# Kernel optimization log

Measured on AMD Instinct MI355X. Metric: run time of the kernel, lower is better.

## Reference

```python
import jax, jax.numpy as jnp
import numpy as np
from functools import partial

B = 1024          # batch of VRP instances
N_CUST = 100      # customers
N = N_CUST + 1    # nodes incl. depot (node 0)
E = 128           # embed_dim
H = 8             # n_heads
DH = E // H       # head depth
CLIP = 10.0
T = 2 * N         # fixed number of decode steps (env.n_nodes * 2)


def setup_inputs() -> dict:
    key = jax.random.key(0)
    ks = jax.random.split(key, 11)
    s = E ** -0.5
    return {
        "depot_xy": jax.random.uniform(ks[0], (B, 2), dtype=jnp.float32),
        "customer_xy": jax.random.uniform(ks[1], (B, N_CUST, 2), dtype=jnp.float32),
        # demands normalized by vehicle capacity (1..9 / 50 for VRP100)
        "demand": jax.random.uniform(ks[2], (B, N_CUST), dtype=jnp.float32, minval=0.02, maxval=0.18),
        "node_embeddings": jax.random.normal(ks[3], (B, N, E), dtype=jnp.float32),
        "graph_embedding": jax.random.normal(ks[4], (B, E), dtype=jnp.float32),
        "Wk1": jax.random.normal(ks[5], (E, E), dtype=jnp.float32) * s,
        "Wv": jax.random.normal(ks[6], (E, E), dtype=jnp.float32) * s,
        "Wk2": jax.random.normal(ks[7], (E, E), dtype=jnp.float32) * s,
        "Wq_fixed": jax.random.normal(ks[8], (E, E), dtype=jnp.float32) * s,
        "Wout": jax.random.normal(ks[9], (E, E), dtype=jnp.float32) * s,
        "Wq_step": jax.random.normal(ks[10], (E + 1, E), dtype=jnp.float32) * s,
    }


def _decode(depot_xy, customer_xy, demand, node_embeddings, graph_embedding,
            Wk1, Wv, Wk2, Wq_fixed, Wout, Wq_step):
    # ---- compute_static ----
    Q_fixed = jnp.einsum('be,ef->bf', graph_embedding, Wq_fixed)[:, None, :]  # [B,1,E]
    K1 = jnp.einsum('bne,ef->bnf', node_embeddings, Wk1)                      # [B,N,E]
    V  = jnp.einsum('bne,ef->bnf', node_embeddings, Wv)
    K2 = jnp.einsum('bne,ef->bnf', node_embeddings, Wk2)
    K1h = K1.reshape(B, N, H, DH)
    Vh  = V.reshape(B, N, H, DH)
    inv_sqrt_dh = 1.0 / np.sqrt(DH)
    inv_sqrt_e = 1.0 / np.sqrt(E)
    bidx = jnp.arange(B)
    NEG = jnp.float32(-1e9)

    def step(carry, _):
        mask, D, prev_node, visited = carry
        # step_context = [embedding of current node, remaining capacity D]
        prev_emb = node_embeddings[bidx, prev_node]                 # [B,E]
        step_context = jnp.concatenate([prev_emb, D], axis=-1)[:, None, :]  # [B,1,E+1]
        # ---- compute_dynamic ----
        Q1 = Q_fixed + jnp.einsum('bqc,cf->bqf', step_context, Wq_step)      # [B,1,E]
        Q1h = Q1.reshape(B, 1, H, DH)
        scores = jnp.einsum('bqhd,bkhd->bhqk', Q1h, K1h) * inv_sqrt_dh       # [B,H,1,N]
        scores = jnp.where(mask[:, None, None, :], NEG, scores)
        attn = jax.nn.softmax(scores, axis=-1)
        glimpse = jnp.einsum('bhqk,bkhd->bqhd', attn, Vh).reshape(B, 1, E)
        Q2 = jnp.einsum('bqe,ef->bqf', glimpse, Wout)                        # [B,1,E]
        logits = CLIP * jnp.tanh(jnp.einsum('bqe,bke->bqk', Q2, K2) * inv_sqrt_e)
        logits = jnp.where(mask[:, None, :], NEG, logits)[:, 0]             # [B,N]
        log_p = jax.nn.log_softmax(logits, axis=-1)
        next_node = jnp.argmax(log_p, axis=-1)                               # greedy decode
        # ---- env._get_step ----
        is_depot = next_node == 0
        cust = jnp.clip(next_node - 1, 0, N_CUST - 1)
        sel_dem = jnp.where(is_depot, 0.0, demand[bidx, cust])
        D_new = jnp.where(is_depot[:, None], 1.0, D - sel_dem[:, None])      # refill at depot
        sel_onehot = (jnp.arange(N_CUST)[None, :] == cust[:, None]) & (~is_depot[:, None])
        visited = visited | sel_onehot
        mask_cust = visited | (demand > D_new)                               # visited or too big
        all_visited = jnp.all(visited, axis=-1)
        mask_depot = is_depot & (~all_visited)                               # can't stay at depot
        mask = jnp.concatenate([mask_depot[:, None], mask_cust], axis=-1)
        return (mask, D_new, next_node, visited), (log_p, next_node)

    mask0 = jnp.concatenate([jnp.ones((B, 1), bool), jnp.zeros((B, N_CUST), bool)], axis=-1)
    D0 = jnp.ones((B, 1), jnp.float32)
    prev0 = jnp.zeros((B,), jnp.int32)
    visited0 = jnp.zeros((B, N_CUST), bool)
    _, (log_ps, tours) = jax.lax.scan(step, (mask0, D0, prev0, visited0), None, length=T)
    log_ps = jnp.transpose(log_ps, (1, 0, 2))   # [B,T,N]
    tours = jnp.transpose(tours, (1, 0))        # [B,T]

    # ---- get_costs ----
    coords = jnp.concatenate([depot_xy[:, None, :], customer_xy], axis=1)    # [B,N,2]
    d = coords[bidx[:, None], tours]                                         # [B,T,2]
    def seglen(v):
        return jnp.sqrt(jnp.sum(v * v, axis=-1) + 1e-10)
    cost = (seglen(d[:, 1:] - d[:, :-1]).sum(-1)
            + seglen(d[:, 0] - depot_xy) + seglen(d[:, -1] - depot_xy))
    # ---- get_log_likelihood ----
    ll = jnp.take_along_axis(log_ps, tours[..., None], axis=-1)[..., 0].sum(-1)
    return cost, ll


def reference(depot_xy, customer_xy, demand, node_embeddings, graph_embedding,
              Wk1, Wv, Wk2, Wq_fixed, Wout, Wq_step):
    return _decode(depot_xy, customer_xy, demand, node_embeddings, graph_embedding,
                   Wk1, Wv, Wk2, Wq_fixed, Wout, Wq_step)
```

## Files before the change

### kernel.cpp

```cpp
#include <hip/hip_runtime.h>
#include <math.h>

#define B_   1024
#define NC   100
#define NN   101
#define E_   128
#define T_   202
#define SVP  132
#define NEGV   -1.0e9
#define GAPTHR 1.0e-3f
#define INVSQE 0.08838834764831845f
#define INVSQED 0.08838834764831845

__device__ __forceinline__ float rdlane(float v, int l) {
    return __int_as_float(__builtin_amdgcn_readlane(__float_as_int(v), l));
}
__device__ __forceinline__ float fast_tanh(float x) {
    float xc = fminf(fmaxf(x, -15.f), 15.f);
    float e  = __expf(2.f * xc);
    return (e - 1.f) / (e + 1.f);
}

__global__ void k_weights(const float* __restrict__ Wk2,
                          const float* __restrict__ Wout,
                          double* __restrict__ M64,
                          float* __restrict__ M32) {
    int g = blockIdx.x;
    int e = threadIdx.x;
    const float* w2 = Wk2 + g * E_;
    const float* wo = Wout + e * E_;
    double acc = 0.0;
#pragma unroll 8
    for (int f = 0; f < E_; ++f) acc += (double)w2[f] * (double)wo[f];
    M64[g * E_ + e] = acc;
    M32[g * E_ + e] = (float)acc;
}

__global__ __launch_bounds__(512, 2)
void k_decode(const float* __restrict__ depot_xy,
              const float* __restrict__ customer_xy,
              const float* __restrict__ demand,
              const float* __restrict__ node_emb,
              const float* __restrict__ graph_emb,
              const float* __restrict__ Wk1,
              const float* __restrict__ Wv,
              const float* __restrict__ Wq_fixed,
              const float* __restrict__ Wq_step,
              const double* __restrict__ M64,
              const float* __restrict__ M32,
              float* __restrict__ out)
{
    __shared__ float  sKs[NN * E_];
    __shared__ __align__(16) float sV[104 * SVP];
    __shared__ double sU[2224];
    __shared__ double sQfix64[E_];
    __shared__ double sWqD64[E_];
    __shared__ float  sQfix32[E_];
    __shared__ float  sWqD32[E_];
    __shared__ float  sCoord[2 * NN];
    __shared__ float  sDem[NC];
    __shared__ float  sD;
    __shared__ double sCost, sLL;
    __shared__ float  sPosX, sPosY;
    __shared__ int    sPrev, sMaskDepot, sTrig, sOvf;
    __shared__ unsigned long long sVis0, sVis1;

    float* fSc = (float*)sU;
    float* gl  = (float*)sU + 832;
    float* fPx = (float*)sU + 960;
    double* dUZ = sU;
    double* dSc = sU + 1024;
    double* dQ1 = sU + 1832;
    double* dGl = sU + 1960;
    double* dVg = sU + 2088;

    const int b      = blockIdx.x;
    const int tid    = threadIdx.x;
    const int lane   = tid & 63;
    const int h      = __builtin_amdgcn_readfirstlane(tid >> 6);
    const int k1     = lane + 64;
    const int k_lane = tid & 127;
    const int q2u    = __builtin_amdgcn_readfirstlane(tid >> 7);
    const int e0     = q2u * 32;

    const float* emb = node_emb + (size_t)b * NN * E_;

    if (tid < E_) {
        const float* ge = graph_emb + (size_t)b * E_;
        double acc = 0.0;
        for (int g = 0; g < E_; ++g)
            acc += (double)ge[g] * (double)Wq_fixed[g * E_ + tid];
        sQfix64[tid] = acc;
        sQfix32[tid] = (float)acc;
        sWqD64[tid]  = (double)Wq_step[128 * E_ + tid];
        sWqD32[tid]  = Wq_step[128 * E_ + tid];
    }
    if (tid < 2 * NN) {
        int k = tid >> 1, xy = tid & 1;
        sCoord[tid] = (k == 0) ? depot_xy[(size_t)b * 2 + xy]
                               : customer_xy[((size_t)b * NC + (k - 1)) * 2 + xy];
    }
    if (tid < NC) sDem[tid] = demand[(size_t)b * NC + tid];
    if (tid == 0) {
        sD = 1.f; sPrev = 0; sVis0 = 0ull; sVis1 = 0ull;
        sMaskDepot = 1; sCost = 0.0; sLL = 0.0; sTrig = 0; sOvf = 0;
        sPosX = depot_xy[(size_t)b * 2 + 0];
        sPosY = depot_xy[(size_t)b * 2 + 1];
    }
    for (int i = tid; i < 3 * SVP; i += 512) sV[101 * SVP + i] = 0.f;

    for (int idx = tid; idx < NN * 32; idx += 512) {
        int k  = idx >> 5;
        int e4 = (idx & 31) * 4;
        const float* er = emb + (size_t)k * E_;
        float4 aV = {0.f, 0.f, 0.f, 0.f};
        float4 aK = {0.f, 0.f, 0.f, 0.f};
        for (int g = 0; g < E_; ++g) {
            float eg = er[g];
            float4 wv = *(const float4*)(Wv      + (size_t)g * E_ + e4);
            float4 wq = *(const float4*)(Wq_step + (size_t)g * E_ + e4);
            aV.x += eg * wv.x; aV.y += eg * wv.y;
            aV.z += eg * wv.z; aV.w += eg * wv.w;
            aK.x += eg * wq.x; aK.y += eg * wq.y;
            aK.z += eg * wq.z; aK.w += eg * wq.w;
        }
        *(float4*)(sV  + (size_t)k * SVP + e4) = aV;
        *(float4*)(sKs + (size_t)k * E_  + e4) = aK;
    }

    float rA[32];
#pragma unroll
    for (int j = 0; j < 32; ++j) rA[j] = 0.f;
    {
        const float* er0 = emb + (size_t)lane * E_;
        const float* er1 = emb + (size_t)((k1 < NN) ? k1 : lane) * E_;
        const float  e1s = (k1 < NN) ? 1.f : 0.f;
        const float* w1b = Wk1 + h * 16;
        for (int g = 0; g < E_; ++g) {
            float a0 = er0[g];
            float a1 = er1[g] * e1s;
            const float* w1 = w1b + (size_t)g * E_;
#pragma unroll
            for (int d = 0; d < 16; ++d) {
                rA[d]      += a0 * w1[d];
                rA[16 + d] += a1 * w1[d];
            }
        }
    }

    float rK2[32];
#pragma unroll
    for (int j = 0; j < 32; ++j) rK2[j] = 0.f;
    if (k_lane < NN) {
        const float* er = emb + (size_t)k_lane * E_;
        for (int g = 0; g < E_; ++g) {
            float eg = er[g];
            const float* mm = M32 + (size_t)g * E_ + e0;
#pragma unroll
            for (int j = 0; j < 32; ++j) rK2[j] += eg * mm[j];
        }
    }
    __syncthreads();

    for (int t = 0; t < T_; ++t) {
        {
            int prev = sPrev;
            float Dv = sD;
            int d_ = h * 16 + (lane & 15);
            float q1v = (sQfix32[d_] + sKs[(size_t)prev * E_ + d_]
                         + Dv * sWqD32[d_]) * 0.25f;

            unsigned long long v0 = sVis0, v1 = sVis1;
            bool mk0, mk1;
            if (lane == 0) mk0 = (sMaskDepot != 0);
            else {
                int c = lane - 1;
                mk0 = ((v0 >> c) & 1ull) || (sDem[c] > Dv);
            }
            if (k1 < NN) {
                int c = k1 - 1;
                bool vis = (c < 64) ? ((v0 >> c) & 1ull)
                                    : ((v1 >> (c - 64)) & 1ull);
                mk1 = vis || (sDem[c] > Dv);
            } else mk1 = true;

            float s0a = 0.f, s0b = 0.f, s1a = 0.f, s1b = 0.f;
#pragma unroll
            for (int d = 0; d < 8; ++d) {
                float qd = rdlane(q1v, d);
                s0a += rA[d] * qd;
                s1a += rA[16 + d] * qd;
            }
#pragma unroll
            for (int d = 8; d < 16; ++d) {
                float qd = rdlane(q1v, d);
                s0b += rA[d] * qd;
                s1b += rA[16 + d] * qd;
            }
            float s0 = s0a + s0b, s1 = s1a + s1b;
            bool ovf = (!mk0 && s0 > 80.f) || (!mk1 && s1 > 80.f);
            if (__any(ovf)) { if (lane == 0) sOvf = 1; }
            float w0 = mk0 ? 0.f : __expf(fminf(s0, 80.f));
            float w1 = mk1 ? 0.f : __expf(fminf(s1, 80.f));
            fSc[h * 104 + lane] = w0;
            if (k1 < 104) fSc[h * 104 + k1] = w1;

            __builtin_amdgcn_wave_barrier();

            int cq4 = lane >> 4;
            const float* sc = fSc + h * 104 + cq4 * 26;
            const float* vv = sV + (size_t)(cq4 * 26) * SVP + d_;
            float p = 0.f, ssum = 0.f;
#pragma unroll
            for (int j = 0; j < 26; ++j) {
                float wgt = sc[j];
                p    += wgt * vv[(size_t)j * SVP];
                ssum += wgt;
            }
            p    += __shfl_xor(p, 16);
            ssum += __shfl_xor(ssum, 16);
            p    += __shfl_xor(p, 32);
            ssum += __shfl_xor(ssum, 32);
            if (lane < 16) gl[d_] = p * (1.0f / ssum);
        }
        __syncthreads();

        {
            int ee = e0 + (tid & 31);
            float glv = gl[ee];
            float xa = 0.f, xb = 0.f, xc = 0.f, xd = 0.f;
#pragma unroll
            for (int j = 0; j < 8; ++j)   xa += rK2[j] * rdlane(glv, j);
#pragma unroll
            for (int j = 8; j < 16; ++j)  xb += rK2[j] * rdlane(glv, j);
#pragma unroll
            for (int j = 16; j < 24; ++j) xc += rK2[j] * rdlane(glv, j);
#pragma unroll
            for (int j = 24; j < 32; ++j) xd += rK2[j] * rdlane(glv, j);
            if (k_lane < NN) fPx[q2u * E_ + k_lane] = (xa + xb) + (xc + xd);
        }
        __syncthreads();

        if (tid < 64) {
            int kA = tid, kB = tid + 64;
            float xA = (fPx[kA] + fPx[128 + kA] + fPx[256 + kA] + fPx[384 + kA]) * INVSQE;
            bool mk1;
            if (kA == 0) mk1 = (sMaskDepot != 0);
            else {
                int c = kA - 1;
                bool vis = (c < 64) ? ((sVis0 >> c) & 1ull) : ((sVis1 >> (c - 64)) & 1ull);
                mk1 = vis || (sDem[c] > sD);
            }
            float xB = -3.0e38f; bool mk2 = true;
            if (kB < NN) {
                xB = (fPx[kB] + fPx[128 + kB] + fPx[256 + kB] + fPx[384 + kB]) * INVSQE;
                int c = kB - 1;
                bool vis = (c < 64) ? ((sVis0 >> c) & 1ull) : ((sVis1 >> (c - 64)) & 1ull);
                mk2 = vis || (sDem[c] > sD);
            }
            float a1v = mk1 ? -3.0e38f : xA;
            float a2v = mk2 ? -3.0e38f : xB;
            float m1; int mi;
            if (a2v > a1v) { m1 = a2v; mi = kB; }
            else           { m1 = a1v; mi = kA; }
            float ls = 0.f;
            if (!mk1)              ls += __expf(10.f * fast_tanh(xA));
            if (kB < NN && !mk2)   ls += __expf(10.f * fast_tanh(xB));
#pragma unroll
            for (int off = 32; off > 0; off >>= 1) {
                float om1 = __shfl_xor(m1, off);
                int   omi = __shfl_xor(mi, off);
                ls += __shfl_xor(ls, off);
                if (om1 > m1 || (om1 == m1 && omi < mi)) { m1 = om1; mi = omi; }
            }
            bool near = false;
            if (!mk1 && kA != mi && a1v > m1 - GAPTHR) near = true;
            if (!mk2 && kB != mi && a2v > m1 - GAPTHR) near = true;
            bool trigAny = __any(near);
            if (tid == 0) {
                bool trig = trigAny || (sOvf != 0) || !(m1 == m1);
                sOvf = 0;
                if (trig) {
                    sTrig = 1;
                } else {
                    float lsel = 10.f * fast_tanh(m1);
                    float logp = lsel - __logf(ls);
                    int nxt = mi;
                    sLL += (double)logp;
                    bool isdep = (nxt == 0);
                    if (isdep) {
                        sD = 1.0f;
                    } else {
                        int c = nxt - 1;
                        sD = sD - sDem[c];
                        if (c < 64) sVis0 |= (1ull << c);
                        else        sVis1 |= (1ull << (c - 64));
                    }
                    bool allv = (sVis0 == 0xFFFFFFFFFFFFFFFFull) &&
                                (sVis1 == 0x0000000FFFFFFFFFull);
                    sMaskDepot = (isdep && !allv) ? 1 : 0;
                    sPrev = nxt;
                    float cx = sCoord[2 * nxt], cy = sCoord[2 * nxt + 1];
                    double dx = (double)cx - (double)sPosX;
                    double dy = (double)cy - (double)sPosY;
                    sCost += sqrt(dx * dx + dy * dy + 1e-10);
                    sPosX = cx; sPosY = cy;
                }
            }
        }
        __syncthreads();

        if (sTrig) {
            if (tid < E_) {
                const float* ep = emb + (size_t)sPrev * E_;
                double ks = 0.0;
                for (int g = 0; g < E_; ++g)
                    ks += (double)ep[g] * (double)Wq_step[(size_t)g * E_ + tid];
                dQ1[tid] = (sQfix64[tid] + ks + (double)sD * sWqD64[tid]) * 0.25;
            }
            __syncthreads();
            for (int idx = tid; idx < 1024; idx += 512) {
                int g = idx >> 3, hh = idx & 7;
                double u = 0.0;
#pragma unroll 4
                for (int d = 0; d < 16; ++d)
                    u += dQ1[hh * 16 + d] * (double)Wk1[(size_t)g * E_ + hh * 16 + d];
                dUZ[idx] = u;
            }
            __syncthreads();
            for (int idx = tid; idx < 1024; idx += 512) {
                int k = idx & 127, hh = idx >> 7;
                if (k < NN) {
                    bool mk;
                    if (k == 0) mk = (sMaskDepot != 0);
                    else {
                        int c = k - 1;
                        bool vis = (c < 64) ? ((sVis0 >> c) & 1ull) : ((sVis1 >> (c - 64)) & 1ull);
                        mk = vis || (sDem[c] > sD);
                    }
                    if (mk) dSc[hh * NN + k] = NEGV;
                    else {
                        const float* ek = emb + (size_t)k * E_;
                        double s = 0.0;
                        for (int g = 0; g < E_; ++g)
                            s += (double)ek[g] * dUZ[g * 8 + hh];
                        dSc[hh * NN + k] = s;
                    }
                }
            }
            __syncthreads();
            {
                int hh = tid >> 6, ln = tid & 63;
                int kA = ln, kB = ln + 64;
                double v1 = dSc[hh * NN + kA];
                double v2 = (kB < NN) ? dSc[hh * NN + kB] : -1.0e300;
                double m = fmax(v1, v2);
#pragma unroll
                for (int off = 32; off > 0; off >>= 1)
                    m = fmax(m, __shfl_xor(m, off));
                double e1 = exp(v1 - m);
                double e2 = (kB < NN) ? exp(v2 - m) : 0.0;
                double s = e1 + e2;
#pragma unroll
                for (int off = 32; off > 0; off >>= 1)
                    s += __shfl_xor(s, off);
                double inv = 1.0 / s;
                dSc[hh * NN + kA] = e1 * inv;
                if (kB < NN) dSc[hh * NN + kB] = e2 * inv;
            }
            __syncthreads();
            for (int idx = tid; idx < 1024; idx += 512) {
                int g = idx >> 3, hh = idx & 7;
                double z = 0.0;
                for (int k = 0; k < NN; ++k)
                    z += dSc[hh * NN + k] * (double)emb[(size_t)k * E_ + g];
                dUZ[idx] = z;
            }
            __syncthreads();
            if (tid < E_) {
                int hh = tid >> 4;
                double g2 = 0.0;
                for (int g = 0; g < E_; ++g)
                    g2 += dUZ[g * 8 + hh] * (double)Wv[(size_t)g * E_ + tid];
                dGl[tid] = g2;
            }
            __syncthreads();
            if (tid < E_) {
                double v = 0.0;
                for (int e = 0; e < E_; ++e)
                    v += dGl[e] * M64[(size_t)tid * E_ + e];
                dVg[tid] = v;
            }
            __syncthreads();
            if (tid < NN) {
                const float* ek = emb + (size_t)tid * E_;
                double x = 0.0;
                for (int g = 0; g < E_; ++g)
                    x += (double)ek[g] * dVg[g];
                dQ1[tid] = x * INVSQED;
            }
            __syncthreads();
            if (tid < 64) {
                int kA = tid, kB = tid + 64;
                double x1 = dQ1[kA];
                bool mk1;
                if (kA == 0) mk1 = (sMaskDepot != 0);
                else {
                    int c = kA - 1;
                    bool vis = (c < 64) ? ((sVis0 >> c) & 1ull) : ((sVis1 >> (c - 64)) & 1ull);
                    mk1 = vis || (sDem[c] > sD);
                }
                double x2 = 0.0; bool mk2 = true;
                if (kB < NN) {
                    x2 = dQ1[kB];
                    int c = kB - 1;
                    bool vis = (c < 64) ? ((sVis0 >> c) & 1ull) : ((sVis1 >> (c - 64)) & 1ull);
                    mk2 = vis || (sDem[c] > sD);
                }
                double a1 = mk1 ? -1.0e300 : x1;
                double a2 = (kB < NN && !mk2) ? x2 : -1.0e300;
                double mv; int mi;
                if (a1 >= a2) { mv = a1; mi = kA; } else { mv = a2; mi = kB; }
#pragma unroll
                for (int off = 32; off > 0; off >>= 1) {
                    double ov = __shfl_xor(mv, off);
                    int    oi = __shfl_xor(mi, off);
                    if (ov > mv || (ov == mv && oi < mi)) { mv = ov; mi = oi; }
                }
                double lmax = 10.0 * tanh(mv);
                double l1 = mk1 ? NEGV : 10.0 * tanh(x1);
                double l2 = (kB < NN) ? (mk2 ? NEGV : 10.0 * tanh(x2)) : 0.0;
                double s = exp(l1 - lmax) + ((kB < NN) ? exp(l2 - lmax) : 0.0);
#pragma unroll
                for (int off = 32; off > 0; off >>= 1)
                    s += __shfl_xor(s, off);
                if (tid == 0) {
                    int nxt = mi;
                    sLL += -log(s);
                    bool isdep = (nxt == 0);
                    if (isdep) {
                        sD = 1.0f;
                    } else {
                        int c = nxt - 1;
                        sD = sD - sDem[c];
                        if (c < 64) sVis0 |= (1ull << c);
                        else        sVis1 |= (1ull << (c - 64));
                    }
                    bool allv = (sVis0 == 0xFFFFFFFFFFFFFFFFull) &&
                                (sVis1 == 0x0000000FFFFFFFFFull);
                    sMaskDepot = (isdep && !allv) ? 1 : 0;
                    sPrev = nxt;
                    float cx = sCoord[2 * nxt], cy = sCoord[2 * nxt + 1];
                    double dx = (double)cx - (double)sPosX;
                    double dy = (double)cy - (double)sPosY;
                    sCost += sqrt(dx * dx + dy * dy + 1e-10);
                    sPosX = cx; sPosY = cy;
                    sTrig = 0;
                }
            }
            __syncthreads();
        }
    }

    if (tid == 0) {
        double dx = (double)sCoord[0] - (double)sPosX;
        double dy = (double)sCoord[1] - (double)sPosY;
        out[b]      = (float)(sCost + sqrt(dx * dx + dy * dy + 1e-10));
        out[B_ + b] = (float)sLL;
    }
}

extern "C" void kernel_launch(void* const* d_in, const int* in_sizes, int n_in,
                              void* d_out, int out_size, void* d_ws, size_t ws_size,
                              hipStream_t stream) {
    const float* depot = (const float*)d_in[0];
    const float* cust  = (const float*)d_in[1];
    const float* dem   = (const float*)d_in[2];
    const float* nemb  = (const float*)d_in[3];
    const float* gemb  = (const float*)d_in[4];
    const float* Wk1   = (const float*)d_in[5];
    const float* Wv    = (const float*)d_in[6];
    const float* Wk2   = (const float*)d_in[7];
    const float* Wqf   = (const float*)d_in[8];
    const float* Wout  = (const float*)d_in[9];
    const float* Wqs   = (const float*)d_in[10];
    float*  out = (float*)d_out;
    double* M64 = (double*)d_ws;
    float*  M32 = (float*)((char*)d_ws + 131072);

    k_weights<<<dim3(128), dim3(128), 0, stream>>>(Wk2, Wout, M64, M32);
    k_decode <<<dim3(B_),  dim3(512), 0, stream>>>(depot, cust, dem, nemb, gemb,
                                                   Wk1, Wv, Wqf, Wqs, M64, M32, out);
}
```

Before: 3.197 ms.

## Shrink LDS footprint to raise occupancy by moving Ks table to global workspace

Moves the per-node Ks projection table out of shared memory into a global workspace buffer and removes the double-precision shared buffers. The rare fp64 fallback step moves into a noinline device function that reuses the sV region as scratch and rebuilds sV afterwards. Launch bounds go from 2 to 4 blocks per CU so more batch blocks can be resident. In exchange, each step now reads Ks from global memory, and the fallback does extra recomputation. The old kernel is kept for when the workspace is too small.

```diff
diff --git a/kernel.cpp b/kernel.cpp
--- a/kernel.cpp
+++ b/kernel.cpp
@@ -36,25 +36,217 @@
     M32[g * E_ + e] = (float)acc;
 }
 
-__global__ __launch_bounds__(512, 2)
-void k_decode(const float* __restrict__ depot_xy,
-              const float* __restrict__ customer_xy,
-              const float* __restrict__ demand,
-              const float* __restrict__ node_emb,
-              const float* __restrict__ graph_emb,
-              const float* __restrict__ Wk1,
-              const float* __restrict__ Wv,
-              const float* __restrict__ Wq_fixed,
-              const float* __restrict__ Wq_step,
-              const double* __restrict__ M64,
-              const float* __restrict__ M32,
-              float* __restrict__ out)
+__device__ __attribute__((noinline)) void fb_step(
+    const float* __restrict__ emb,
+    const float* __restrict__ gemb_b,
+    const float* __restrict__ Wk1,
+    const float* __restrict__ Wv,
+    const float* __restrict__ Wq_fixed,
+    const float* __restrict__ Wq_step,
+    const double* __restrict__ M64,
+    float* sV,
+    const float* sDem, const float* sCoord,
+    float* sD, int* sPrev, int* sMaskDepot,
+    unsigned long long* sVis0, unsigned long long* sVis1,
+    double* sCost, double* sLL, float* sPosX, float* sPosY,
+    int* sTrig, int tid)
 {
-    __shared__ float  sKs[NN * E_];
+    double* dUZ = (double*)sV;
+    double* dSc = dUZ + 1024;
+    double* dQ1 = dUZ + 1832;
+    double* dGl = dUZ + 1960;
+    double* dVg = dUZ + 2088;
+
+    if (tid < E_) {
+        double qf = 0.0, ks = 0.0;
+        const float* ep = emb + (size_t)(*sPrev) * E_;
+#pragma clang loop unroll(disable)
+        for (int g = 0; g < E_; ++g) {
+            qf += (double)gemb_b[g] * (double)Wq_fixed[(size_t)g * E_ + tid];
+            ks += (double)ep[g]     * (double)Wq_step[(size_t)g * E_ + tid];
+        }
+        dQ1[tid] = (qf + ks + (double)(*sD) * (double)Wq_step[128 * E_ + tid]) * 0.25;
+    }
+    __syncthreads();
+    for (int idx = tid; idx < 1024; idx += 512) {
+        int g = idx >> 3, hh = idx & 7;
+        double u = 0.0;
+#pragma clang loop unroll(disable)
+        for (int d = 0; d < 16; ++d)
+            u += dQ1[hh * 16 + d] * (double)Wk1[(size_t)g * E_ + hh * 16 + d];
+        dUZ[idx] = u;
+    }
+    __syncthreads();
+    for (int idx = tid; idx < 1024; idx += 512) {
+        int k = idx & 127, hh = idx >> 7;
+        if (k < NN) {
+            bool mk;
+            if (k == 0) mk = (*sMaskDepot != 0);
+            else {
+                int c = k - 1;
+                bool vis = (c < 64) ? ((*sVis0 >> c) & 1ull) : ((*sVis1 >> (c - 64)) & 1ull);
+                mk = vis || (sDem[c] > *sD);
+            }
+            if (mk) dSc[hh * NN + k] = NEGV;
+            else {
+                const float* ek = emb + (size_t)k * E_;
+                double s = 0.0;
+#pragma clang loop unroll(disable)
+                for (int g = 0; g < E_; ++g)
+                    s += (double)ek[g] * dUZ[g * 8 + hh];
+                dSc[hh * NN + k] = s;
+            }
+        }
+    }
+    __syncthreads();
+    {
+        int hh = tid >> 6, ln = tid & 63;
+        int kA = ln, kB = ln + 64;
+        double v1 = dSc[hh * NN + kA];
+        double v2 = (kB < NN) ? dSc[hh * NN + kB] : -1.0e300;
+        double m = fmax(v1, v2);
+#pragma unroll
+        for (int off = 32; off > 0; off >>= 1)
+            m = fmax(m, __shfl_xor(m, off));
+        double e1 = exp(v1 - m);
+        double e2 = (kB < NN) ? exp(v2 - m) : 0.0;
+        double s = e1 + e2;
+#pragma unroll
+        for (int off = 32; off > 0; off >>= 1)
+            s += __shfl_xor(s, off);
+        double inv = 1.0 / s;
+        dSc[hh * NN + kA] = e1 * inv;
+        if (kB < NN) dSc[hh * NN + kB] = e2 * inv;
+    }
+    __syncthreads();
+    for (int idx = tid; idx < 1024; idx += 512) {
+        int g = idx >> 3, hh = idx & 7;
+        double z = 0.0;
+#pragma clang loop unroll(disable)
+        for (int k = 0; k < NN; ++k)
+            z += dSc[hh * NN + k] * (double)emb[(size_t)k * E_ + g];
+        dUZ[idx] = z;
+    }
+    __syncthreads();
+    if (tid < E_) {
+        int hh = tid >> 4;
+        double g2 = 0.0;
+#pragma clang loop unroll(disable)
+        for (int g = 0; g < E_; ++g)
+            g2 += dUZ[g * 8 + hh] * (double)Wv[(size_t)g * E_ + tid];
+        dGl[tid] = g2;
+    }
+    __syncthreads();
+    if (tid < E_) {
+        double v = 0.0;
+#pragma clang loop unroll(disable)
+        for (int e = 0; e < E_; ++e)
+            v += dGl[e] * M64[(size_t)tid * E_ + e];
+        dVg[tid] = v;
+    }
+    __syncthreads();
+    if (tid < NN) {
+        const float* ek = emb + (size_t)tid * E_;
+        double x = 0.0;
+#pragma clang loop unroll(disable)
+        for (int g = 0; g < E_; ++g)
+            x += (double)ek[g] * dVg[g];
+        dQ1[tid] = x * INVSQED;
+    }
+    __syncthreads();
+    if (tid < 64) {
+        int kA = tid, kB = tid + 64;
+        double x1 = dQ1[kA];
+        bool mk1;
+        if (kA == 0) mk1 = (*sMaskDepot != 0);
+        else {
+            int c = kA - 1;
+            bool vis = (c < 64) ? ((*sVis0 >> c) & 1ull) : ((*sVis1 >> (c - 64)) & 1ull);
+            mk1 = vis || (sDem[c] > *sD);
+        }
+        double x2 = 0.0; bool mk2 = true;
+        if (kB < NN) {
+            x2 = dQ1[kB];
+            int c = kB - 1;
+            bool vis = (c < 64) ? ((*sVis0 >> c) & 1ull) : ((*sVis1 >> (c - 64)) & 1ull);
+            mk2 = vis || (sDem[c] > *sD);
+        }
+        double a1 = mk1 ? -1.0e300 : x1;
+        double a2 = (kB < NN && !mk2) ? x2 : -1.0e300;
+        double mv; int mi;
+        if (a1 >= a2) { mv = a1; mi = kA; } else { mv = a2; mi = kB; }
+#pragma unroll
+        for (int off = 32; off > 0; off >>= 1) {
+            double ov = __shfl_xor(mv, off);
+            int    oi = __shfl_xor(mi, off);
+            if (ov > mv || (ov == mv && oi < mi)) { mv = ov; mi = oi; }
+        }
+        double lmax = 10.0 * tanh(mv);
+        double l1 = mk1 ? NEGV : 10.0 * tanh(x1);
+        double l2 = (kB < NN) ? (mk2 ? NEGV : 10.0 * tanh(x2)) : 0.0;
+        double s = exp(l1 - lmax) + ((kB < NN) ? exp(l2 - lmax) : 0.0);
+#pragma unroll
+        for (int off = 32; off > 0; off >>= 1)
+            s += __shfl_xor(s, off);
+        if (tid == 0) {
+            int nxt = mi;
+            *sLL += -log(s);
+            bool isdep = (nxt == 0);
+            if (isdep) {
+                *sD = 1.0f;
+            } else {
+                int c = nxt - 1;
+                *sD = *sD - sDem[c];
+                if (c < 64) *sVis0 |= (1ull << c);
+                else        *sVis1 |= (1ull << (c - 64));
+            }
+            bool allv = (*sVis0 == 0xFFFFFFFFFFFFFFFFull) &&
+                        (*sVis1 == 0x0000000FFFFFFFFFull);
+            *sMaskDepot = (isdep && !allv) ? 1 : 0;
+            *sPrev = nxt;
+            float cx = sCoord[2 * nxt], cy = sCoord[2 * nxt + 1];
+            double dx = (double)cx - (double)(*sPosX);
+            double dy = (double)cy - (double)(*sPosY);
+            *sCost += sqrt(dx * dx + dy * dy + 1e-10);
+            *sPosX = cx; *sPosY = cy;
+            *sTrig = 0;
+        }
+    }
+    __syncthreads();
+
+    for (int idx = tid; idx < NN * 32; idx += 512) {
+        int k  = idx >> 5;
+        int e4 = (idx & 31) * 4;
+        const float* er = emb + (size_t)k * E_;
+        float4 aV = {0.f, 0.f, 0.f, 0.f};
+#pragma clang loop unroll(disable)
+        for (int g = 0; g < E_; ++g) {
+            float eg = er[g];
+            float4 wv = *(const float4*)(Wv + (size_t)g * E_ + e4);
+            aV.x += eg * wv.x; aV.y += eg * wv.y;
+            aV.z += eg * wv.z; aV.w += eg * wv.w;
+        }
+        *(float4*)(sV + (size_t)k * SVP + e4) = aV;
+    }
+}
+
+__global__ __launch_bounds__(512, 4)
+void k_decode_g(const float* __restrict__ depot_xy,
+                const float* __restrict__ customer_xy,
+                const float* __restrict__ demand,
+                const float* __restrict__ node_emb,
+                const float* __restrict__ graph_emb,
+                const float* __restrict__ Wk1,
+                const float* __restrict__ Wv,
+                const float* __restrict__ Wq_fixed,
+                const float* __restrict__ Wq_step,
+                const double* __restrict__ M64,
+                const float* __restrict__ M32,
+                float* __restrict__ gks,
+                float* __restrict__ out)
+{
     __shared__ __align__(16) float sV[104 * SVP];
-    __shared__ double sU[2224];
-    __shared__ double sQfix64[E_];
-    __shared__ double sWqD64[E_];
+    __shared__ float  sF[1472];
     __shared__ float  sQfix32[E_];
     __shared__ float  sWqD32[E_];
     __shared__ float  sCoord[2 * NN];
@@ -65,14 +257,9 @@
     __shared__ int    sPrev, sMaskDepot, sTrig, sOvf;
     __shared__ unsigned long long sVis0, sVis1;
 
-    float* fSc = (float*)sU;
-    float* gl  = (float*)sU + 832;
-    float* fPx = (float*)sU + 960;
-    double* dUZ = sU;
-    double* dSc = sU + 1024;
-    double* dQ1 = sU + 1832;
-    double* dGl = sU + 1960;
-    double* dVg = sU + 2088;
+    float* fSc = sF;
+    float* gl  = sF + 832;
+    float* fPx = sF + 960;
 
     const int b      = blockIdx.x;
     const int tid    = threadIdx.x;
@@ -83,16 +270,14 @@
     const int q2u    = __builtin_amdgcn_readfirstlane(tid >> 7);
     const int e0     = q2u * 32;
 
-    const float* emb = node_emb + (size_t)b * NN * E_;
+    const float* emb    = node_emb + (size_t)b * NN * E_;
+    const float* gemb_b = graph_emb + (size_t)b * E_;
 
     if (tid < E_) {
-        const float* ge = graph_emb + (size_t)b * E_;
         double acc = 0.0;
         for (int g = 0; g < E_; ++g)
-            acc += (double)ge[g] * (double)Wq_fixed[g * E_ + tid];
-        sQfix64[tid] = acc;
+            acc += (double)gemb_b[g] * (double)Wq_fixed[g * E_ + tid];
         sQfix32[tid] = (float)acc;
-        sWqD64[tid]  = (double)Wq_step[128 * E_ + tid];
         sWqD32[tid]  = Wq_step[128 * E_ + tid];
     }
     if (tid < 2 * NN) {
@@ -124,8 +309,8 @@
             aK.x += eg * wq.x; aK.y += eg * wq.y;
             aK.z += eg * wq.z; aK.w += eg * wq.w;
         }
-        *(float4*)(sV  + (size_t)k * SVP + e4) = aV;
-        *(float4*)(sKs + (size_t)k * E_  + e4) = aK;
+        *(float4*)(sV + (size_t)k * SVP + e4) = aV;
+        *(float4*)(gks + ((size_t)b * NN + k) * E_ + e4) = aK;
     }
 
     float rA[32];
@@ -167,8 +352,8 @@
             int prev = sPrev;
             float Dv = sD;
             int d_ = h * 16 + (lane & 15);
-            float q1v = (sQfix32[d_] + sKs[(size_t)prev * E_ + d_]
-                         + Dv * sWqD32[d_]) * 0.25f;
+            float ksv = gks[((size_t)b * NN + prev) * E_ + d_];
+            float q1v = (sQfix32[d_] + ksv + Dv * sWqD32[d_]) * 0.25f;
 
             unsigned long long v0 = sVis0, v1 = sVis1;
             bool mk0, mk1;
@@ -311,132 +496,264 @@
         __syncthreads();
 
         if (sTrig) {
-            if (tid < E_) {
-                const float* ep = emb + (size_t)sPrev * E_;
-                double ks = 0.0;
-                for (int g = 0; g < E_; ++g)
-                    ks += (double)ep[g] * (double)Wq_step[(size_t)g * E_ + tid];
-                dQ1[tid] = (sQfix64[tid] + ks + (double)sD * sWqD64[tid]) * 0.25;
-            }
+            fb_step(emb, gemb_b, Wk1, Wv, Wq_fixed, Wq_step, M64,
+                    sV, sDem, sCoord, &sD, &sPrev, &sMaskDepot,
+                    &sVis0, &sVis1, &sCost, &sLL, &sPosX, &sPosY,
+                    &sTrig, tid);
             __syncthreads();
-            for (int idx = tid; idx < 1024; idx += 512) {
-                int g = idx >> 3, hh = idx & 7;
-                double u = 0.0;
-#pragma unroll 4
-                for (int d = 0; d < 16; ++d)
-                    u += dQ1[hh * 16 + d] * (double)Wk1[(size_t)g * E_ + hh * 16 + d];
-                dUZ[idx] = u;
-            }
-            __syncthreads();
-            for (int idx = tid; idx < 1024; idx += 512) {
-                int k = idx & 127, hh = idx >> 7;
-                if (k < NN) {
-                    bool mk;
-                    if (k == 0) mk = (sMaskDepot != 0);
-                    else {
-                        int c = k - 1;
-                        bool vis = (c < 64) ? ((sVis0 >> c) & 1ull) : ((sVis1 >> (c - 64)) & 1ull);
-                        mk = vis || (sDem[c] > sD);
-                    }
-                    if (mk) dSc[hh * NN + k] = NEGV;
-                    else {
-                        const float* ek = emb + (size_t)k * E_;
-                        double s = 0.0;
-                        for (int g = 0; g < E_; ++g)
-                            s += (double)ek[g] * dUZ[g * 8 + hh];
-                        dSc[hh * NN + k] = s;
-                    }
-                }
-            }
-            __syncthreads();
-            {
-                int hh = tid >> 6, ln = tid & 63;
-                int kA = ln, kB = ln + 64;
-                double v1 = dSc[hh * NN + kA];
-                double v2 = (kB < NN) ? dSc[hh * NN + kB] : -1.0e300;
-                double m = fmax(v1, v2);
-#pragma unroll
-                for (int off = 32; off > 0; off >>= 1)
-                    m = fmax(m, __shfl_xor(m, off));
-                double e1 = exp(v1 - m);
-                double e2 = (kB < NN) ? exp(v2 - m) : 0.0;
-                double s = e1 + e2;
-#pragma unroll
-                for (int off = 32; off > 0; off >>= 1)
-                    s += __shfl_xor(s, off);
-                double inv = 1.0 / s;
-                dSc[hh * NN + kA] = e1 * inv;
-                if (kB < NN) dSc[hh * NN + kB] = e2 * inv;
-            }
-            __syncthreads();
-            for (int idx = tid; idx < 1024; idx += 512) {
-                int g = idx >> 3, hh = idx & 7;
-                double z = 0.0;
-                for (int k = 0; k < NN; ++k)
-                    z += dSc[hh * NN + k] * (double)emb[(size_t)k * E_ + g];
-                dUZ[idx] = z;
-            }
-            __syncthreads();
-            if (tid < E_) {
-                int hh = tid >> 4;
-                double g2 = 0.0;
-                for (int g = 0; g < E_; ++g)
-                    g2 += dUZ[g * 8 + hh] * (double)Wv[(size_t)g * E_ + tid];
-                dGl[tid] = g2;
-            }
-            __syncthreads();
-            if (tid < E_) {
-                double v = 0.0;
-                for (int e = 0; e < E_; ++e)
-                    v += dGl[e] * M64[(size_t)tid * E_ + e];
-                dVg[tid] = v;
-            }
-            __syncthreads();
-            if (tid < NN) {
-                const float* ek = emb + (size_t)tid * E_;
-                double x = 0.0;
-                for (int g = 0; g < E_; ++g)
-                    x += (double)ek[g] * dVg[g];
-                dQ1[tid] = x * INVSQED;
-            }
-            __syncthreads();
-            if (tid < 64) {
-                int kA = tid, kB = tid + 64;
-                double x1 = dQ1[kA];
-                bool mk1;
-                if (kA == 0) mk1 = (sMaskDepot != 0);
-                else {
-                    int c = kA - 1;
-                    bool vis = (c < 64) ? ((sVis0 >> c) & 1ull) : ((sVis1 >> (c - 64)) & 1ull);
-                    mk1 = vis || (sDem[c] > sD);
-                }
-                double x2 = 0.0; bool mk2 = true;
-                if (kB < NN) {
-                    x2 = dQ1[kB];
-                    int c = kB - 1;
-                    bool vis = (c < 64) ? ((sVis0 >> c) & 1ull) : ((sVis1 >> (c - 64)) & 1ull);
-                    mk2 = vis || (sDem[c] > sD);
-                }
-                double a1 = mk1 ? -1.0e300 : x1;
-                double a2 = (kB < NN && !mk2) ? x2 : -1.0e300;
-                double mv; int mi;
-                if (a1 >= a2) { mv = a1; mi = kA; } else { mv = a2; mi = kB; }
-#pragma unroll
-                for (int off = 32; off > 0; off >>= 1) {
-                    double ov = __shfl_xor(mv, off);
-                    int    oi = __shfl_xor(mi, off);
-                    if (ov > mv || (ov == mv && oi < mi)) { mv = ov; mi = oi; }
-                }
-                double lmax = 10.0 * tanh(mv);
-                double l1 = mk1 ? NEGV : 10.0 * tanh(x1);
-                double l2 = (kB < NN) ? (mk2 ? NEGV : 10.0 * tanh(x2)) : 0.0;
-                double s = exp(l1 - lmax) + ((kB < NN) ? exp(l2 - lmax) : 0.0);
-#pragma unroll
-                for (int off = 32; off > 0; off >>= 1)
-                    s += __shfl_xor(s, off);
-                if (tid == 0) {
+        }
+    }
+
+    if (tid == 0) {
+        double dx = (double)sCoord[0] - (double)sPosX;
+        double dy = (double)sCoord[1] - (double)sPosY;
+        out[b]      = (float)(sCost + sqrt(dx * dx + dy * dy + 1e-10));
+        out[B_ + b] = (float)sLL;
+    }
+}
+
+__global__ __launch_bounds__(512, 2)
+void k_decode_l(const float* __restrict__ depot_xy,
+                const float* __restrict__ customer_xy,
+                const float* __restrict__ demand,
+                const float* __restrict__ node_emb,
+                const float* __restrict__ graph_emb,
+                const float* __restrict__ Wk1,
+                const float* __restrict__ Wv,
+                const float* __restrict__ Wq_fixed,
+                const float* __restrict__ Wq_step,
+                const double* __restrict__ M64,
+                const float* __restrict__ M32,
+                float* __restrict__ out)
+{
+    __shared__ float  sKs[NN * E_];
+    __shared__ __align__(16) float sV[104 * SVP];
+    __shared__ float  sF[1472];
+    __shared__ float  sQfix32[E_];
+    __shared__ float  sWqD32[E_];
+    __shared__ float  sCoord[2 * NN];
+    __shared__ float  sDem[NC];
+    __shared__ float  sD;
+    __shared__ double sCost, sLL;
+    __shared__ float  sPosX, sPosY;
+    __shared__ int    sPrev, sMaskDepot, sTrig, sOvf;
+    __shared__ unsigned long long sVis0, sVis1;
+
+    float* fSc = sF;
+    float* gl  = sF + 832;
+    float* fPx = sF + 960;
+
+    const int b      = blockIdx.x;
+    const int tid    = threadIdx.x;
+    const int lane   = tid & 63;
+    const int h      = __builtin_amdgcn_readfirstlane(tid >> 6);
+    const int k1     = lane + 64;
+    const int k_lane = tid & 127;
+    const int q2u    = __builtin_amdgcn_readfirstlane(tid >> 7);
+    const int e0     = q2u * 32;
+
+    const float* emb    = node_emb + (size_t)b * NN * E_;
+    const float* gemb_b = graph_emb + (size_t)b * E_;
+
+    if (tid < E_) {
+        double acc = 0.0;
+        for (int g = 0; g < E_; ++g)
+            acc += (double)gemb_b[g] * (double)Wq_fixed[g * E_ + tid];
+        sQfix32[tid] = (float)acc;
+        sWqD32[tid]  = Wq_step[128 * E_ + tid];
+    }
+    if (tid < 2 * NN) {
+        int k = tid >> 1, xy = tid & 1;
+        sCoord[tid] = (k == 0) ? depot_xy[(size_t)b * 2 + xy]
+                               : customer_xy[((size_t)b * NC + (k - 1)) * 2 + xy];
+    }
+    if (tid < NC) sDem[tid] = demand[(size_t)b * NC + tid];
+    if (tid == 0) {
+        sD = 1.f; sPrev = 0; sVis0 = 0ull; sVis1 = 0ull;
+        sMaskDepot = 1; sCost = 0.0; sLL = 0.0; sTrig = 0; sOvf = 0;
+        sPosX = depot_xy[(size_t)b * 2 + 0];
+        sPosY = depot_xy[(size_t)b * 2 + 1];
+    }
+    for (int i = tid; i < 3 * SVP; i += 512) sV[101 * SVP + i] = 0.f;
+
+    for (int idx = tid; idx < NN * 32; idx += 512) {
+        int k  = idx >> 5;
+        int e4 = (idx & 31) * 4;
+        const float* er = emb + (size_t)k * E_;
+        float4 aV = {0.f, 0.f, 0.f, 0.f};
+        float4 aK = {0.f, 0.f, 0.f, 0.f};
+        for (int g = 0; g < E_; ++g) {
+            float eg = er[g];
+            float4 wv = *(const float4*)(Wv      + (size_t)g * E_ + e4);
+            float4 wq = *(const float4*)(Wq_step + (size_t)g * E_ + e4);
+            aV.x += eg * wv.x; aV.y += eg * wv.y;
+            aV.z += eg * wv.z; aV.w += eg * wv.w;
+            aK.x += eg * wq.x; aK.y += eg * wq.y;
+            aK.z += eg * wq.z; aK.w += eg * wq.w;
+        }
+        *(float4*)(sV  + (size_t)k * SVP + e4) = aV;
+        *(float4*)(sKs + (size_t)k * E_  + e4) = aK;
+    }
+
+    float rA[32];
+#pragma unroll
+    for (int j = 0; j < 32; ++j) rA[j] = 0.f;
+    {
+        const float* er0 = emb + (size_t)lane * E_;
+        const float* er1 = emb + (size_t)((k1 < NN) ? k1 : lane) * E_;
+        const float  e1s = (k1 < NN) ? 1.f : 0.f;
+        const float* w1b = Wk1 + h * 16;
+        for (int g = 0; g < E_; ++g) {
+            float a0 = er0[g];
+            float a1 = er1[g] * e1s;
+            const float* w1 = w1b + (size_t)g * E_;
+#pragma unroll
+            for (int d = 0; d < 16; ++d) {
+                rA[d]      += a0 * w1[d];
+                rA[16 + d] += a1 * w1[d];
+            }
+        }
+    }
+
+    float rK2[32];
+#pragma unroll
+    for (int j = 0; j < 32; ++j) rK2[j] = 0.f;
+    if (k_lane < NN) {
+        const float* er = emb + (size_t)k_lane * E_;
+        for (int g = 0; g < E_; ++g) {
+            float eg = er[g];
+            const float* mm = M32 + (size_t)g * E_ + e0;
+#pragma unroll
+            for (int j = 0; j < 32; ++j) rK2[j] += eg * mm[j];
+        }
+    }
+    __syncthreads();
+
+    for (int t = 0; t < T_; ++t) {
+        {
+            int prev = sPrev;
+            float Dv = sD;
+            int d_ = h * 16 + (lane & 15);
+            float q1v = (sQfix32[d_] + sKs[(size_t)prev * E_ + d_]
+                         + Dv * sWqD32[d_]) * 0.25f;
+
+            unsigned long long v0 = sVis0, v1 = sVis1;
+            bool mk0, mk1;
+            if (lane == 0) mk0 = (sMaskDepot != 0);
+            else {
+                int c = lane - 1;
+                mk0 = ((v0 >> c) & 1ull) || (sDem[c] > Dv);
+            }
+            if (k1 < NN) {
+                int c = k1 - 1;
+                bool vis = (c < 64) ? ((v0 >> c) & 1ull)
+                                    : ((v1 >> (c - 64)) & 1ull);
+                mk1 = vis || (sDem[c] > Dv);
+            } else mk1 = true;
+
+            float s0a = 0.f, s0b = 0.f, s1a = 0.f, s1b = 0.f;
+#pragma unroll
+            for (int d = 0; d < 8; ++d) {
+                float qd = rdlane(q1v, d);
+                s0a += rA[d] * qd;
+                s1a += rA[16 + d] * qd;
+            }
+#pragma unroll
+            for (int d = 8; d < 16; ++d) {
+                float qd = rdlane(q1v, d);
+                s0b += rA[d] * qd;
+                s1b += rA[16 + d] * qd;
+            }
+            float s0 = s0a + s0b, s1 = s1a + s1b;
+            bool ovf = (!mk0 && s0 > 80.f) || (!mk1 && s1 > 80.f);
+            if (__any(ovf)) { if (lane == 0) sOvf = 1; }
+            float w0 = mk0 ? 0.f : __expf(fminf(s0, 80.f));
+            float w1 = mk1 ? 0.f : __expf(fminf(s1, 80.f));
+            fSc[h * 104 + lane] = w0;
+            if (k1 < 104) fSc[h * 104 + k1] = w1;
+
+            __builtin_amdgcn_wave_barrier();
+
+            int cq4 = lane >> 4;
+            const float* sc = fSc + h * 104 + cq4 * 26;
+            const float* vv = sV + (size_t)(cq4 * 26) * SVP + d_;
+            float p = 0.f, ssum = 0.f;
+#pragma unroll
+            for (int j = 0; j < 26; ++j) {
+                float wgt = sc[j];
+                p    += wgt * vv[(size_t)j * SVP];
+                ssum += wgt;
+            }
+            p    += __shfl_xor(p, 16);
+            ssum += __shfl_xor(ssum, 16);
+            p    += __shfl_xor(p, 32);
+            ssum += __shfl_xor(ssum, 32);
+            if (lane < 16) gl[d_] = p * (1.0f / ssum);
+        }
+        __syncthreads();
+
+        {
+            int ee = e0 + (tid & 31);
+            float glv = gl[ee];
+            float xa = 0.f, xb = 0.f, xc = 0.f, xd = 0.f;
+#pragma unroll
+            for (int j = 0; j < 8; ++j)   xa += rK2[j] * rdlane(glv, j);
+#pragma unroll
+            for (int j = 8; j < 16; ++j)  xb += rK2[j] * rdlane(glv, j);
+#pragma unroll
+            for (int j = 16; j < 24; ++j) xc += rK2[j] * rdlane(glv, j);
+#pragma unroll
+            for (int j = 24; j < 32; ++j) xd += rK2[j] * rdlane(glv, j);
+            if (k_lane < NN) fPx[q2u * E_ + k_lane] = (xa + xb) + (xc + xd);
+        }
+        __syncthreads();
+
+        if (tid < 64) {
+            int kA = tid, kB = tid + 64;
+            float xA = (fPx[kA] + fPx[128 + kA] + fPx[256 + kA] + fPx[384 + kA]) * INVSQE;
+            bool mk1;
+            if (kA == 0) mk1 = (sMaskDepot != 0);
+            else {
+                int c = kA - 1;
+                bool vis = (c < 64) ? ((sVis0 >> c) & 1ull) : ((sVis1 >> (c - 64)) & 1ull);
+                mk1 = vis || (sDem[c] > sD);
+            }
+            float xB = -3.0e38f; bool mk2 = true;
+            if (kB < NN) {
+                xB = (fPx[kB] + fPx[128 + kB] + fPx[256 + kB] + fPx[384 + kB]) * INVSQE;
+                int c = kB - 1;
+                bool vis = (c < 64) ? ((sVis0 >> c) & 1ull) : ((sVis1 >> (c - 64)) & 1ull);
+                mk2 = vis || (sDem[c] > sD);
+            }
+            float a1v = mk1 ? -3.0e38f : xA;
+            float a2v = mk2 ? -3.0e38f : xB;
+            float m1; int mi;
+            if (a2v > a1v) { m1 = a2v; mi = kB; }
+            else           { m1 = a1v; mi = kA; }
+            float ls = 0.f;
+            if (!mk1)              ls += __expf(10.f * fast_tanh(xA));
+            if (kB < NN && !mk2)   ls += __expf(10.f * fast_tanh(xB));
+#pragma unroll
+            for (int off = 32; off > 0; off >>= 1) {
+                float om1 = __shfl_xor(m1, off);
+                int   omi = __shfl_xor(mi, off);
+                ls += __shfl_xor(ls, off);
+                if (om1 > m1 || (om1 == m1 && omi < mi)) { m1 = om1; mi = omi; }
+            }
+            bool near = false;
+            if (!mk1 && kA != mi && a1v > m1 - GAPTHR) near = true;
+            if (!mk2 && kB != mi && a2v > m1 - GAPTHR) near = true;
+            bool trigAny = __any(near);
+            if (tid == 0) {
+                bool trig = trigAny || (sOvf != 0) || !(m1 == m1);
+                sOvf = 0;
+                if (trig) {
+                    sTrig = 1;
+                } else {
+                    float lsel = 10.f * fast_tanh(m1);
+                    float logp = lsel - __logf(ls);
                     int nxt = mi;
-                    sLL += -log(s);
+                    sLL += (double)logp;
                     bool isdep = (nxt == 0);
                     if (isdep) {
                         sD = 1.0f;
@@ -455,9 +772,16 @@
                     double dy = (double)cy - (double)sPosY;
                     sCost += sqrt(dx * dx + dy * dy + 1e-10);
                     sPosX = cx; sPosY = cy;
-                    sTrig = 0;
                 }
             }
+        }
+        __syncthreads();
+
+        if (sTrig) {
+            fb_step(emb, gemb_b, Wk1, Wv, Wq_fixed, Wq_step, M64,
+                    sV, sDem, sCoord, &sD, &sPrev, &sMaskDepot,
+                    &sVis0, &sVis1, &sCost, &sLL, &sPosX, &sPosY,
+                    &sTrig, tid);
             __syncthreads();
         }
     }
@@ -485,10 +809,23 @@
     const float* Wout  = (const float*)d_in[9];
     const float* Wqs   = (const float*)d_in[10];
     float*  out = (float*)d_out;
+
     double* M64 = (double*)d_ws;
     float*  M32 = (float*)((char*)d_ws + 131072);
 
+    const size_t gks_off   = 196608;
+    const size_t gks_bytes = (size_t)B_ * NN * E_ * sizeof(float);
+    float* gks = (ws_size >= gks_off + gks_bytes)
+               ? (float*)((char*)d_ws + gks_off) : nullptr;
+
     k_weights<<<dim3(128), dim3(128), 0, stream>>>(Wk2, Wout, M64, M32);
-    k_decode <<<dim3(B_),  dim3(512), 0, stream>>>(depot, cust, dem, nemb, gemb,
-                                                   Wk1, Wv, Wqf, Wqs, M64, M32, out);
+    if (gks) {
+        k_decode_g<<<dim3(B_), dim3(512), 0, stream>>>(depot, cust, dem, nemb,
+                                                       gemb, Wk1, Wv, Wqf, Wqs,
+                                                       M64, M32, gks, out);
+    } else {
+        k_decode_l<<<dim3(B_), dim3(512), 0, stream>>>(depot, cust, dem, nemb,
+                                                       gemb, Wk1, Wv, Wqf, Wqs,
+                                                       M64, M32, out);
+    }
 }
```

Measured after the change: 6.109 ms. 91.1% more time.

## Fuse K2 projection into per-head attention wave, remove one block barrier per step

Applied to the files above, without the earlier changes.

The second-stage logit projection is re-partitioned so each head's wave holds K2 slices for its own 16 dimensions across both node halves. It then computes the partial logits directly from its glimpse values through readlane, without first writing the glimpse to shared memory. This removes a shared-memory round trip and one __syncthreads per decode step. The cost is that the final reduction now sums eight partials per node instead of four, and the precompute loop carries more registers.

```diff
diff --git a/kernel.cpp b/kernel.cpp
--- a/kernel.cpp
+++ b/kernel.cpp
@@ -65,9 +65,8 @@
     __shared__ int    sPrev, sMaskDepot, sTrig, sOvf;
     __shared__ unsigned long long sVis0, sVis1;
 
-    float* fSc = (float*)sU;
-    float* gl  = (float*)sU + 832;
-    float* fPx = (float*)sU + 960;
+    float* fSc  = (float*)sU;
+    float* fPx8 = (float*)sU + 832;
     double* dUZ = sU;
     double* dSc = sU + 1024;
     double* dQ1 = sU + 1832;
@@ -79,9 +78,6 @@
     const int lane   = tid & 63;
     const int h      = __builtin_amdgcn_readfirstlane(tid >> 6);
     const int k1     = lane + 64;
-    const int k_lane = tid & 127;
-    const int q2u    = __builtin_amdgcn_readfirstlane(tid >> 7);
-    const int e0     = q2u * 32;
 
     const float* emb = node_emb + (size_t)b * NN * E_;
 
@@ -128,36 +124,27 @@
         *(float4*)(sKs + (size_t)k * E_  + e4) = aK;
     }
 
-    float rA[32];
-#pragma unroll
-    for (int j = 0; j < 32; ++j) rA[j] = 0.f;
+    float rA[32], rK2[32];
+#pragma unroll
+    for (int j = 0; j < 32; ++j) { rA[j] = 0.f; rK2[j] = 0.f; }
     {
         const float* er0 = emb + (size_t)lane * E_;
         const float* er1 = emb + (size_t)((k1 < NN) ? k1 : lane) * E_;
         const float  e1s = (k1 < NN) ? 1.f : 0.f;
         const float* w1b = Wk1 + h * 16;
+        const float* m2b = M32 + h * 16;
         for (int g = 0; g < E_; ++g) {
             float a0 = er0[g];
             float a1 = er1[g] * e1s;
             const float* w1 = w1b + (size_t)g * E_;
+            const float* mm = m2b + (size_t)g * E_;
 #pragma unroll
             for (int d = 0; d < 16; ++d) {
-                rA[d]      += a0 * w1[d];
-                rA[16 + d] += a1 * w1[d];
-            }
-        }
-    }
-
-    float rK2[32];
-#pragma unroll
-    for (int j = 0; j < 32; ++j) rK2[j] = 0.f;
-    if (k_lane < NN) {
-        const float* er = emb + (size_t)k_lane * E_;
-        for (int g = 0; g < E_; ++g) {
-            float eg = er[g];
-            const float* mm = M32 + (size_t)g * E_ + e0;
-#pragma unroll
-            for (int j = 0; j < 32; ++j) rK2[j] += eg * mm[j];
+                rA[d]       += a0 * w1[d];
+                rA[16 + d]  += a1 * w1[d];
+                rK2[d]      += a0 * mm[d];
+                rK2[16 + d] += a1 * mm[d];
+            }
         }
     }
     __syncthreads();
@@ -221,29 +208,26 @@
             ssum += __shfl_xor(ssum, 16);
             p    += __shfl_xor(p, 32);
             ssum += __shfl_xor(ssum, 32);
-            if (lane < 16) gl[d_] = p * (1.0f / ssum);
+            float glval = p * (1.0f / ssum);
+
+            float x0 = 0.f, x1 = 0.f;
+#pragma unroll
+            for (int d = 0; d < 16; ++d) {
+                float gd = rdlane(glval, d);
+                x0 += rK2[d] * gd;
+                x1 += rK2[16 + d] * gd;
+            }
+            fPx8[h * E_ + lane] = x0;
+            if (k1 < NN) fPx8[h * E_ + k1] = x1;
         }
         __syncthreads();
 
-        {
-            int ee = e0 + (tid & 31);
-            float glv = gl[ee];
-            float xa = 0.f, xb = 0.f, xc = 0.f, xd = 0.f;
-#pragma unroll
-            for (int j = 0; j < 8; ++j)   xa += rK2[j] * rdlane(glv, j);
-#pragma unroll
-            for (int j = 8; j < 16; ++j)  xb += rK2[j] * rdlane(glv, j);
-#pragma unroll
-            for (int j = 16; j < 24; ++j) xc += rK2[j] * rdlane(glv, j);
-#pragma unroll
-            for (int j = 24; j < 32; ++j) xd += rK2[j] * rdlane(glv, j);
-            if (k_lane < NN) fPx[q2u * E_ + k_lane] = (xa + xb) + (xc + xd);
-        }
-        __syncthreads();
-
         if (tid < 64) {
             int kA = tid, kB = tid + 64;
-            float xA = (fPx[kA] + fPx[128 + kA] + fPx[256 + kA] + fPx[384 + kA]) * INVSQE;
+            float xA = 0.f, xB = -3.0e38f;
+#pragma unroll
+            for (int hh = 0; hh < 8; ++hh) xA += fPx8[hh * E_ + kA];
+            xA *= INVSQE;
             bool mk1;
             if (kA == 0) mk1 = (sMaskDepot != 0);
             else {
@@ -251,9 +235,12 @@
                 bool vis = (c < 64) ? ((sVis0 >> c) & 1ull) : ((sVis1 >> (c - 64)) & 1ull);
                 mk1 = vis || (sDem[c] > sD);
             }
-            float xB = -3.0e38f; bool mk2 = true;
+            bool mk2 = true;
             if (kB < NN) {
-                xB = (fPx[kB] + fPx[128 + kB] + fPx[256 + kB] + fPx[384 + kB]) * INVSQE;
+                float xs = 0.f;
+#pragma unroll
+                for (int hh = 0; hh < 8; ++hh) xs += fPx8[hh * E_ + kB];
+                xB = xs * INVSQE;
                 int c = kB - 1;
                 bool vis = (c < 64) ? ((sVis0 >> c) & 1ull) : ((sVis1 >> (c - 64)) & 1ull);
                 mk2 = vis || (sDem[c] > sD);
```

Result: faster. 3.130 ms (-2.1%).
